# Performance work log

Hardware: AMD Instinct MI355X
Metric: run time of the kernel (lower is better)

The kernel has to match this reference:

```python
import jax, jax.numpy as jnp
import numpy as np

D = 1024

def setup_inputs() -> dict:
    key = jax.random.key(0)
    ks = jax.random.split(key, 7)
    s = 1.0 / np.sqrt(D)
    return {
        "x": jax.random.normal(ks[0], (8, 2048, D), dtype=jnp.float32),
        "Wq": jax.random.uniform(ks[1], (D, D), jnp.float32, -s, s),
        "bq": jax.random.uniform(ks[2], (D,), jnp.float32, -s, s),
        "Wk": jax.random.uniform(ks[3], (D, D), jnp.float32, -s, s),
        "bk": jax.random.uniform(ks[4], (D,), jnp.float32, -s, s),
        "Wv": jax.random.uniform(ks[5], (D, D), jnp.float32, -s, s),
        "bv": jax.random.uniform(ks[6], (D,), jnp.float32, -s, s),
    }

def reference(x, Wq, bq, Wk, bk, Wv, bv):
    # torch Linear: y = x @ W.T + b
    Q = jnp.einsum('bsd,ed->bse', x, Wq) + bq
    K = jnp.einsum('bsd,ed->bse', x, Wk) + bk
    V = jnp.einsum('bsd,ed->bse', x, Wv) + bv
    scores = jnp.einsum('bse,bte->bst', Q, K) / jnp.sqrt(jnp.float32(x.shape[-1]))
    weights = jax.nn.softmax(scores, axis=-1)
    out = jnp.einsum('bst,bte->bse', weights, V)
    return jnp.mean(out, axis=0)
```

## Files before the change

### kernel.cpp

```cpp
#include <hip/hip_runtime.h>

typedef unsigned short u16;
typedef __attribute__((ext_vector_type(8))) short s16x8;
typedef __attribute__((ext_vector_type(4))) short s16x4;
typedef __attribute__((ext_vector_type(4))) float f32x4;

typedef const __attribute__((address_space(1))) void gas_void;
typedef __attribute__((address_space(3))) void las_void;

__device__ inline u16 f2bf(float f){
  union { float f; unsigned u; } c; c.f = f;
  unsigned r = c.u + 0x7fffu + ((c.u >> 16) & 1u);
  return (u16)(r >> 16);
}
__device__ inline float bf2f(u16 b){
  union { unsigned u; float f; } c; c.u = ((unsigned)b) << 16;
  return c.f;
}

extern "C" __global__ __launch_bounds__(256) void cvt_f32_bf16(
    const float* __restrict__ src, u16* __restrict__ dst, int n4){
  int stride = gridDim.x * blockDim.x;
  for (int i = blockIdx.x * blockDim.x + threadIdx.x; i < n4; i += stride){
    float4 f = reinterpret_cast<const float4*>(src)[i];
    s16x4 o;
    o[0] = (short)f2bf(f.x); o[1] = (short)f2bf(f.y);
    o[2] = (short)f2bf(f.z); o[3] = (short)f2bf(f.w);
    reinterpret_cast<s16x4*>(dst)[i] = o;
  }
}

extern "C" __global__ __launch_bounds__(256) void cvt_w3(
    const float* __restrict__ w0, const float* __restrict__ w1,
    const float* __restrict__ w2, u16* __restrict__ dst, int n4each){
  int stride = gridDim.x * blockDim.x;
  int total = 3 * n4each;
  for (int i = blockIdx.x * blockDim.x + threadIdx.x; i < total; i += stride){
    int w = i / n4each, off = i - w * n4each;
    const float* src = w == 0 ? w0 : w == 1 ? w1 : w2;
    float4 f = reinterpret_cast<const float4*>(src)[off];
    s16x4 o;
    o[0] = (short)f2bf(f.x); o[1] = (short)f2bf(f.y);
    o[2] = (short)f2bf(f.z); o[3] = (short)f2bf(f.w);
    reinterpret_cast<s16x4*>(dst)[i] = o;
  }
}

extern "C" __global__ __launch_bounds__(256) void reduce8(
    const float* __restrict__ p, float* __restrict__ out, int n4, long stride4){
  int gs = gridDim.x * blockDim.x;
  for (int i = blockIdx.x * blockDim.x + threadIdx.x; i < n4; i += gs){
    float4 a = reinterpret_cast<const float4*>(p)[i];
    #pragma unroll
    for (int z = 1; z < 8; ++z){
      float4 b = reinterpret_cast<const float4*>(p)[i + z * stride4];
      a.x += b.x; a.y += b.y; a.z += b.z; a.w += b.w;
    }
    reinterpret_cast<float4*>(out)[i] = a;
  }
}

#define BM 256
#define BN 256
#define BK 64

__device__ inline void stage256(const u16* __restrict__ g, int ld, int row0, int k0,
                                u16* lds, int tid){
  const int wave = tid >> 6;
  #pragma unroll
  for (int j = 0; j < 4; ++j){
    int c = j * 512 + tid;
    int row = c >> 3, sch = c & 7;
    int ch = sch ^ (row & 7);
    const u16* src = g + (long)(row0 + row) * ld + k0 + ch * 8;
    u16* dst = lds + (size_t)(j * 512 + wave * 64) * 8;
    __builtin_amdgcn_global_load_lds((gas_void*)src, (las_void*)dst, 16, 0, 0);
  }
}

template<int EPI>
__global__ __launch_bounds__(512, 2) void gemm256(
    const u16* __restrict__ A, const u16* __restrict__ B, void* __restrict__ C,
    const float* __restrict__ bias, float scale, int K,
    int lda, int ldb, int ldc, long sAz, long sBz, long sCz)
{
  __shared__ u16 As[2][BM * BK];
  __shared__ u16 Bs[2][BN * BK];
  const int tid = threadIdx.x;
  const int lane = tid & 63, wave = tid >> 6;
  const int wm = (wave >> 2) * 128, wn = (wave & 3) * 64;

  const int gx = gridDim.x;
  const int nwg = gx * gridDim.y;
  const int hw = blockIdx.y * gx + blockIdx.x;
  const int lg = (hw & 7) * (nwg >> 3) + (hw >> 3);
  const int pr  = lg / (2 * gx);
  const int rem = lg - pr * 2 * gx;
  const int bm = (pr * 2 + (rem & 1)) * BM;
  const int bn = (rem >> 1) * BN;
  const int z = blockIdx.z;
  A += (long)z * sAz; B += (long)z * sBz;

  f32x4 acc[8][4];
  #pragma unroll
  for (int i = 0; i < 8; ++i)
    #pragma unroll
    for (int j = 0; j < 4; ++j) acc[i][j] = (f32x4){0.f, 0.f, 0.f, 0.f};

  const int lrow = lane & 15, lkg = lane >> 4;
  const int nt = K >> 6;

  auto compute = [&](const u16* as, const u16* bs){
    __builtin_amdgcn_s_setprio(1);
    #pragma unroll
    for (int kk = 0; kk < 2; ++kk){
      s16x8 bfr[4];
      #pragma unroll
      for (int j = 0; j < 4; ++j){
        int row = wn + j * 16 + lrow;
        int ch = (kk * 4 + lkg) ^ (row & 7);
        bfr[j] = *reinterpret_cast<const s16x8*>(
            reinterpret_cast<const char*>(bs) + row * 128 + ch * 16);
      }
      #pragma unroll
      for (int i = 0; i < 8; ++i){
        int row = wm + i * 16 + lrow;
        int ch = (kk * 4 + lkg) ^ (row & 7);
        s16x8 af = *reinterpret_cast<const s16x8*>(
            reinterpret_cast<const char*>(as) + row * 128 + ch * 16);
        #pragma unroll
        for (int j = 0; j < 4; ++j)
          acc[i][j] = __builtin_amdgcn_mfma_f32_16x16x32_bf16(af, bfr[j], acc[i][j], 0, 0, 0);
      }
    }
    __builtin_amdgcn_s_setprio(0);
  };

  stage256(A, lda, bm, 0, As[0], tid);
  stage256(B, ldb, bn, 0, Bs[0], tid);

  for (int t = 0; t < nt - 1; ++t){
    int nb = (t + 1) & 1;
    stage256(A, lda, bm, (t + 1) << 6, As[nb], tid);
    stage256(B, ldb, bn, (t + 1) << 6, Bs[nb], tid);
    asm volatile("s_waitcnt vmcnt(8)" ::: "memory");
    __builtin_amdgcn_s_barrier();
    asm volatile("" ::: "memory");
    compute(As[t & 1], Bs[t & 1]);
    asm volatile("" ::: "memory");
    __builtin_amdgcn_s_barrier();
    asm volatile("" ::: "memory");
  }
  asm volatile("s_waitcnt vmcnt(0)" ::: "memory");
  __builtin_amdgcn_s_barrier();
  asm volatile("" ::: "memory");
  compute(As[(nt - 1) & 1], Bs[(nt - 1) & 1]);

  #pragma unroll
  for (int i = 0; i < 8; ++i){
    #pragma unroll
    for (int j = 0; j < 4; ++j){
      #pragma unroll
      for (int r = 0; r < 4; ++r){
        int row = bm + wm + i * 16 + lkg * 4 + r;
        int col = bn + wn + j * 16 + lrow;
        float v = acc[i][j][r] * scale;
        if (EPI == 0){
          if (bias) v += bias[col];
          reinterpret_cast<u16*>(C)[(long)z * sCz + (long)row * ldc + col] = f2bf(v);
        } else if (EPI == 1){
          if (bias) v += bias[col];
          int b = row >> 11, tt = row & 2047;
          reinterpret_cast<u16*>(C)[((long)b << 21) + ((long)col << 11) + tt] = f2bf(v);
        } else {
          reinterpret_cast<float*>(C)[(long)z * sCz + (long)row * ldc + col] = v;
        }
      }
    }
  }
}

extern "C" __global__ __launch_bounds__(256) void softmax_rows(u16* __restrict__ S){
  long row = blockIdx.x;
  u16* p = S + row * 2048;
  int tid = threadIdx.x;
  s16x8 vv = reinterpret_cast<s16x8*>(p)[tid];
  float v[8];
  float m = -3.4e38f;
  #pragma unroll
  for (int j = 0; j < 8; ++j){ v[j] = bf2f((u16)vv[j]); m = fmaxf(m, v[j]); }
  #pragma unroll
  for (int o = 32; o; o >>= 1) m = fmaxf(m, __shfl_xor(m, o));
  __shared__ float sm[4], ss[4];
  int wave = tid >> 6, lane = tid & 63;
  if (lane == 0) sm[wave] = m;
  __syncthreads();
  m = fmaxf(fmaxf(sm[0], sm[1]), fmaxf(sm[2], sm[3]));
  float e[8], s = 0.f;
  #pragma unroll
  for (int j = 0; j < 8; ++j){ e[j] = __expf(v[j] - m); s += e[j]; }
  #pragma unroll
  for (int o = 32; o; o >>= 1) s += __shfl_xor(s, o);
  if (lane == 0) ss[wave] = s;
  __syncthreads();
  s = ss[0] + ss[1] + ss[2] + ss[3];
  float inv = 1.0f / s;
  s16x8 ov;
  #pragma unroll
  for (int j = 0; j < 8; ++j) ov[j] = (short)f2bf(e[j] * inv);
  reinterpret_cast<s16x8*>(p)[tid] = ov;
}

extern "C" void kernel_launch(void* const* d_in, const int* in_sizes, int n_in,
                              void* d_out, int out_size, void* d_ws, size_t ws_size,
                              hipStream_t stream){
  const float* x  = (const float*)d_in[0];
  const float* Wq = (const float*)d_in[1];
  const float* bq = (const float*)d_in[2];
  const float* Wk = (const float*)d_in[3];
  const float* bk = (const float*)d_in[4];
  const float* Wv = (const float*)d_in[5];
  const float* bv = (const float*)d_in[6];

  const long NX = 16384L * 1024;
  const long NW = 1024L * 1024;
  const long NS = 8L * 2048 * 2048;

  u16* xbf = (u16*)d_ws;
  u16* Wb  = xbf + NX;
  u16* Qb  = Wb + 3 * NW;
  u16* Kb  = Qb + NX;
  u16* Vtb = Kb + NX;
  u16* S   = Vtb + NX;

  float* partial = (float*)Qb;

  size_t need = (size_t)(NX + 3 * NW + 3 * NX + NS) * 2;
  if (ws_size < need) return;

  cvt_f32_bf16<<<2048, 256, 0, stream>>>(x, xbf, (int)(NX / 4));
  cvt_w3<<<768, 256, 0, stream>>>(Wq, Wk, Wv, Wb, (int)(NW / 4));

  gemm256<0><<<dim3(4, 64, 1), 512, 0, stream>>>(
      xbf, Wb,          Qb,  bq, 1.f, 1024, 1024, 1024, 1024, 0, 0, 0);
  gemm256<0><<<dim3(4, 64, 1), 512, 0, stream>>>(
      xbf, Wb + NW,     Kb,  bk, 1.f, 1024, 1024, 1024, 1024, 0, 0, 0);
  gemm256<1><<<dim3(4, 64, 1), 512, 0, stream>>>(
      xbf, Wb + 2 * NW, Vtb, bv, 1.f, 1024, 1024, 1024, 0,    0, 0, 0);

  gemm256<0><<<dim3(8, 8, 8), 512, 0, stream>>>(
      Qb, Kb, S, nullptr, 0.03125f, 1024, 1024, 1024, 2048,
      2048L * 1024, 2048L * 1024, 2048L * 2048);

  softmax_rows<<<8 * 2048, 256, 0, stream>>>(S);

  gemm256<2><<<dim3(4, 8, 8), 512, 0, stream>>>(
      S, Vtb, partial, nullptr, 0.125f, 2048, 2048, 2048, 1024,
      2048L * 2048, 1024L * 2048, 2048L * 1024);

  reduce8<<<1024, 256, 0, stream>>>(
      partial, (float*)d_out, (int)(2048L * 1024 / 4), 2048L * 1024 / 4);
}
```

Before: 378.4 us.

## Split GEMM main loop into four barrier-separated load/MFMA phases with interleaved prefetch

Replaces the single compute-per-tile loop with four phases per K-tile. Each phase loads a half set of A/B fragments from LDS, issues part of the next tile's global-to-LDS prefetch, and runs a 4x4 MFMA block at raised priority. Barriers between phases are meant to keep waves in lockstep, so LDS reads, global loads and MFMA work from co-resident waves overlap better. It adds many more barriers per tile and waits for the prefetch within the same iteration, which may reduce latency hiding.

```diff
diff --git a/kernel.cpp b/kernel.cpp
--- a/kernel.cpp
+++ b/kernel.cpp
@@ -78,6 +78,19 @@
   }
 }
 
+#define BARRIER() do { asm volatile("" ::: "memory"); \
+                       __builtin_amdgcn_s_barrier();  \
+                       asm volatile("" ::: "memory"); } while (0)
+
+#define MFMA16(RO) do { __builtin_amdgcn_s_setprio(1);                         \
+    _Pragma("unroll")                                                          \
+    for (int i_ = 0; i_ < 4; ++i_)                                             \
+      _Pragma("unroll")                                                        \
+      for (int j_ = 0; j_ < 4; ++j_)                                           \
+        acc[(RO) + i_][j_] = __builtin_amdgcn_mfma_f32_16x16x32_bf16(          \
+            af[i_], bfr[j_], acc[(RO) + i_][j_], 0, 0, 0);                     \
+    __builtin_amdgcn_s_setprio(0); } while (0)
+
 template<int EPI>
 __global__ __launch_bounds__(512, 2) void gemm256(
     const u16* __restrict__ A, const u16* __restrict__ B, void* __restrict__ C,
@@ -110,51 +123,63 @@
   const int lrow = lane & 15, lkg = lane >> 4;
   const int nt = K >> 6;
 
-  auto compute = [&](const u16* as, const u16* bs){
-    __builtin_amdgcn_s_setprio(1);
-    #pragma unroll
-    for (int kk = 0; kk < 2; ++kk){
-      s16x8 bfr[4];
-      #pragma unroll
-      for (int j = 0; j < 4; ++j){
-        int row = wn + j * 16 + lrow;
-        int ch = (kk * 4 + lkg) ^ (row & 7);
-        bfr[j] = *reinterpret_cast<const s16x8*>(
-            reinterpret_cast<const char*>(bs) + row * 128 + ch * 16);
-      }
-      #pragma unroll
-      for (int i = 0; i < 8; ++i){
-        int row = wm + i * 16 + lrow;
-        int ch = (kk * 4 + lkg) ^ (row & 7);
-        s16x8 af = *reinterpret_cast<const s16x8*>(
-            reinterpret_cast<const char*>(as) + row * 128 + ch * 16);
-        #pragma unroll
-        for (int j = 0; j < 4; ++j)
-          acc[i][j] = __builtin_amdgcn_mfma_f32_16x16x32_bf16(af, bfr[j], acc[i][j], 0, 0, 0);
-      }
-    }
-    __builtin_amdgcn_s_setprio(0);
+  auto lda4 = [&](s16x8* d, const u16* base, int ih, int kk){
+    #pragma unroll
+    for (int i = 0; i < 4; ++i){
+      int row = wm + (ih * 4 + i) * 16 + lrow;
+      int ch = (kk * 4 + lkg) ^ (row & 7);
+      d[i] = *reinterpret_cast<const s16x8*>(
+          reinterpret_cast<const char*>(base) + row * 128 + ch * 16);
+    }
+  };
+  auto ldb4 = [&](s16x8* d, const u16* base, int kk){
+    #pragma unroll
+    for (int j = 0; j < 4; ++j){
+      int row = wn + j * 16 + lrow;
+      int ch = (kk * 4 + lkg) ^ (row & 7);
+      d[j] = *reinterpret_cast<const s16x8*>(
+          reinterpret_cast<const char*>(base) + row * 128 + ch * 16);
+    }
   };
 
   stage256(A, lda, bm, 0, As[0], tid);
   stage256(B, ldb, bn, 0, Bs[0], tid);
-
-  for (int t = 0; t < nt - 1; ++t){
-    int nb = (t + 1) & 1;
-    stage256(A, lda, bm, (t + 1) << 6, As[nb], tid);
-    stage256(B, ldb, bn, (t + 1) << 6, Bs[nb], tid);
-    asm volatile("s_waitcnt vmcnt(8)" ::: "memory");
-    __builtin_amdgcn_s_barrier();
-    asm volatile("" ::: "memory");
-    compute(As[t & 1], Bs[t & 1]);
-    asm volatile("" ::: "memory");
-    __builtin_amdgcn_s_barrier();
-    asm volatile("" ::: "memory");
-  }
   asm volatile("s_waitcnt vmcnt(0)" ::: "memory");
-  __builtin_amdgcn_s_barrier();
-  asm volatile("" ::: "memory");
-  compute(As[(nt - 1) & 1], Bs[(nt - 1) & 1]);
+  BARRIER();
+
+  for (int t = 0; t < nt; ++t){
+    const int cur = t & 1, nxt = cur ^ 1;
+    const bool pf = (t + 1) < nt;
+    const int k1 = (t + 1) << 6;
+    const u16* as = As[cur];
+    const u16* bs = Bs[cur];
+    s16x8 af[4], bfr[4];
+
+    ldb4(bfr, bs, 0);
+    lda4(af, as, 0, 0);
+    if (pf) stage256(A, lda, bm, k1, As[nxt], tid);
+    BARRIER();
+    MFMA16(0);
+    BARRIER();
+
+    lda4(af, as, 1, 0);
+    if (pf) stage256(B, ldb, bn, k1, Bs[nxt], tid);
+    BARRIER();
+    MFMA16(4);
+    BARRIER();
+
+    ldb4(bfr, bs, 1);
+    lda4(af, as, 0, 1);
+    BARRIER();
+    MFMA16(0);
+    BARRIER();
+
+    lda4(af, as, 1, 1);
+    if (pf) asm volatile("s_waitcnt vmcnt(0)" ::: "memory");
+    BARRIER();
+    MFMA16(4);
+    BARRIER();
+  }
 
   #pragma unroll
   for (int i = 0; i < 8; ++i){
```

After: 360.4 us. 4.8% less time.
